# Kernel tuning notes

Hardware: AMD Instinct MI355X
Metric: run time of the kernel (lower is better)

## Reference

```python
import jax, jax.numpy as jnp
import numpy as np

# --- static Cayley table for Cl(3) (8 blades) ---
def _derive_cayley_table():
    basis_gens = [(), (1,), (2,), (3,), (1, 2), (1, 3), (2, 3), (1, 2, 3)]
    gens_to_idx = {g: i for i, g in enumerate(basis_gens)}
    def reduce(a, b):
        gens = list(a) + list(b)
        sign = 1
        changed = True
        while changed:
            changed = False
            i = 0
            while i < len(gens) - 1:
                if gens[i] == gens[i + 1]:
                    gens.pop(i); gens.pop(i)
                    changed = True
                    if i > 0:
                        i -= 1
                elif gens[i] > gens[i + 1]:
                    gens[i], gens[i + 1] = gens[i + 1], gens[i]
                    sign *= -1
                    changed = True
                    i += 1
                else:
                    i += 1
        return gens_to_idx[tuple(gens)], sign
    return [[reduce(basis_gens[i], basis_gens[j]) for j in range(8)] for i in range(8)]

_TAB = _derive_cayley_table()
SI = np.array([i for i in range(8) for _ in range(8)], dtype=np.int32)
SJ = np.array([j for _ in range(8) for j in range(8)], dtype=np.int32)
TK = np.array([_TAB[i][j][0] for i in range(8) for j in range(8)], dtype=np.int32)
SG = np.array([float(_TAB[i][j][1]) for i in range(8) for j in range(8)], dtype=np.float32)

N_TOK, N_BLADE, D_BLADE, D_FFN = 8192, 8, 256, 1024
LN_EPS = 1e-5


def setup_inputs() -> dict:
    key = jax.random.key(0)
    ks = jax.random.split(key, 5)
    scale = 0.02
    return {
        'x': jax.random.normal(ks[0], (N_TOK, N_BLADE, D_BLADE), jnp.float32),
        'interaction_weights': jnp.full((64,), 0.1, jnp.float32),
        'geo_gate': jnp.asarray(0.5, jnp.float32),
        'ln_w': jnp.ones((D_BLADE,), jnp.float32),
        'ln_b': jnp.zeros((D_BLADE,), jnp.float32),
        'W_gate': jax.random.normal(ks[1], (D_BLADE, D_FFN), jnp.float32) * scale,
        'W_up': jax.random.normal(ks[2], (D_BLADE, D_FFN), jnp.float32) * scale,
        'W_down': jax.random.normal(ks[3], (D_FFN, D_BLADE), jnp.float32) * scale,
    }


def reference(x, interaction_weights, geo_gate, ln_w, ln_b, W_gate, W_up, W_down):
    si = jnp.asarray(SI); sj = jnp.asarray(SJ); tk = jnp.asarray(TK)
    sg = jnp.asarray(SG).astype(x.dtype)
    w = jax.nn.sigmoid(interaction_weights).astype(x.dtype)
    # gather blade pairs, weighted Cayley product: (N, 64, D)
    products = x[:, si, :] * x[:, sj, :] * (sg * w)[None, :, None]
    # scatter-add into target blades: (N, 8, D)
    geo = jnp.zeros_like(x).at[:, tk, :].add(products)
    g = jax.nn.sigmoid(geo_gate)
    mixed = g * geo + (1.0 - g) * x
    # LayerNorm over D
    flat = mixed.reshape(-1, x.shape[-1])
    mu = jnp.mean(flat, axis=-1, keepdims=True)
    var = jnp.var(flat, axis=-1, keepdims=True)
    flat = (flat - mu) * jax.lax.rsqrt(var + LN_EPS) * ln_w + ln_b
    # SwiGLU FFN
    h = jax.nn.silu(flat @ W_gate) * (flat @ W_up)
    out = (h @ W_down).reshape(x.shape)
    return x + out
```

## Files before the change

### kernel.cpp

```cpp
#include <hip/hip_runtime.h>
#include <hip/hip_bf16.h>

typedef __bf16 bf16x8 __attribute__((ext_vector_type(8)));
typedef float floatx4 __attribute__((ext_vector_type(4)));

constexpr int TK[64] = {
  0,1,2,3,4,5,6,7,
  1,0,4,5,2,3,7,6,
  2,4,0,6,1,7,3,5,
  3,5,6,0,7,1,2,4,
  4,2,1,7,0,6,5,3,
  5,3,7,1,6,0,4,2,
  6,7,3,2,5,4,0,1,
  7,6,5,4,3,2,1,0
};
constexpr float SGN[64] = {
  1, 1, 1, 1, 1, 1, 1, 1,
  1, 1, 1, 1, 1, 1, 1, 1,
  1,-1, 1, 1,-1,-1, 1,-1,
  1,-1,-1, 1, 1,-1,-1, 1,
  1,-1, 1, 1,-1,-1, 1,-1,
  1,-1,-1, 1, 1,-1,-1, 1,
  1, 1,-1, 1,-1, 1,-1,-1,
  1, 1,-1, 1,-1, 1,-1,-1
};

__device__ __forceinline__ void async16(const void* g, void* l) {
  __builtin_amdgcn_global_load_lds(
      (const __attribute__((address_space(1))) void*)g,
      (__attribute__((address_space(3))) void*)l, 16, 0, 0);
}

__global__ __launch_bounds__(256) void transpose_cast(
    const float* __restrict__ src, __bf16* __restrict__ dst, int K, int N)
{
  __shared__ float s[32 * 33];
  const int t = threadIdx.x;
  const int k0 = blockIdx.y * 32, n0 = blockIdx.x * 32;
  const int r = t >> 5, c = t & 31;
  #pragma unroll
  for (int i = 0; i < 4; ++i)
    s[(r + i * 8) * 33 + c] = src[(size_t)(k0 + r + i * 8) * N + n0 + c];
  __syncthreads();
  #pragma unroll
  for (int i = 0; i < 4; ++i)
    dst[(size_t)(n0 + r + i * 8) * K + k0 + c] = (__bf16)s[c * 33 + r + i * 8];
}

__global__ __launch_bounds__(256) void geo_ln(
    const float* __restrict__ X,
    const float* __restrict__ IW,
    const float* __restrict__ GG,
    const float* __restrict__ LW, const float* __restrict__ LB,
    __bf16* __restrict__ F)
{
  __shared__ float sw[64];
  __shared__ float smix[8 * 256];
  __shared__ float sstat[16];
  const int t = threadIdx.x;
  const int tok = blockIdx.x;

  if (t < 64) sw[t] = SGN[t] / (1.f + __expf(-IW[t]));

  float xv[8];
  #pragma unroll
  for (int b = 0; b < 8; ++b) xv[b] = X[(size_t)tok * 2048 + b * 256 + t];
  const float g = 1.f / (1.f + __expf(-GG[0]));

  __syncthreads();

  float geo[8] = {0.f, 0.f, 0.f, 0.f, 0.f, 0.f, 0.f, 0.f};
  #pragma unroll
  for (int p = 0; p < 64; ++p)
    geo[TK[p]] += xv[p >> 3] * xv[p & 7] * sw[p];

  float mv[8];
  #pragma unroll
  for (int b = 0; b < 8; ++b) {
    mv[b] = g * geo[b] + (1.f - g) * xv[b];
    smix[b * 256 + t] = mv[b];
  }
  __syncthreads();

  const int wv = t >> 6, lane = t & 63;
  #pragma unroll
  for (int s = 0; s < 2; ++s) {
    int b = wv * 2 + s;
    float v0 = smix[b * 256 + lane];
    float v1 = smix[b * 256 + 64 + lane];
    float v2 = smix[b * 256 + 128 + lane];
    float v3 = smix[b * 256 + 192 + lane];
    float sum = v0 + v1 + v2 + v3;
    float sq  = v0*v0 + v1*v1 + v2*v2 + v3*v3;
    #pragma unroll
    for (int off = 32; off > 0; off >>= 1) {
      sum += __shfl_xor(sum, off, 64);
      sq  += __shfl_xor(sq,  off, 64);
    }
    if (lane == 0) {
      float mu  = sum * (1.f / 256.f);
      float var = sq * (1.f / 256.f) - mu * mu;
      sstat[b]     = mu;
      sstat[8 + b] = rsqrtf(var + 1e-5f);
    }
  }
  __syncthreads();

  const float lw = LW[t], lb = LB[t];
  #pragma unroll
  for (int b = 0; b < 8; ++b) {
    float v = (mv[b] - sstat[b]) * sstat[8 + b] * lw + lb;
    F[(size_t)(tok * 8 + b) * 256 + t] = (__bf16)v;
  }
}

__global__ __launch_bounds__(256, 3) void gemm_gateup(
    const __bf16* __restrict__ A,
    const __bf16* __restrict__ Bg,
    const __bf16* __restrict__ Bu,
    __bf16* __restrict__ H)
{
  __shared__ __bf16 sA[128 * 64];
  __shared__ __bf16 sBg[64 * 64];
  __shared__ __bf16 sBu[64 * 64];
  const int t = threadIdx.x;
  const int f0 = blockIdx.x * 64;
  const int m0 = blockIdx.y * 128;
  const int lane = t & 63, wv = t >> 6;
  const int wm = wv & 1, wf = wv >> 1;
  const int l15 = lane & 15, quad = lane >> 4;

  int aoff[4], boff[2];
  #pragma unroll
  for (int i = 0; i < 4; ++i) {
    int idx = i * 256 + t, row = idx >> 3, slot = idx & 7;
    aoff[i] = (m0 + row) * 256 + (slot ^ (row & 7)) * 8;
  }
  #pragma unroll
  for (int i = 0; i < 2; ++i) {
    int idx = i * 256 + t, row = idx >> 3, slot = idx & 7;
    boff[i] = (f0 + row) * 256 + (slot ^ (row & 7)) * 8;
  }

  floatx4 zero = {0.f, 0.f, 0.f, 0.f};
  floatx4 accg[4][2], accu[4][2];
  #pragma unroll
  for (int i = 0; i < 4; ++i)
    #pragma unroll
    for (int j = 0; j < 2; ++j) { accg[i][j] = zero; accu[i][j] = zero; }

  const int xr = l15 & 7;
  for (int k = 0; k < 4; ++k) {
    const int kk = k * 64;
    #pragma unroll
    for (int i = 0; i < 4; ++i) async16(A + aoff[i] + kk, &sA[(i * 256 + t) * 8]);
    #pragma unroll
    for (int i = 0; i < 2; ++i) {
      async16(Bg + boff[i] + kk, &sBg[(i * 256 + t) * 8]);
      async16(Bu + boff[i] + kk, &sBu[(i * 256 + t) * 8]);
    }
    __syncthreads();

    #pragma unroll
    for (int s = 0; s < 2; ++s) {
      const int slot = (s * 4 + quad) ^ xr;
      bf16x8 av[4], bg[2], bu[2];
      #pragma unroll
      for (int i = 0; i < 4; ++i) {
        int r = wm * 64 + i * 16 + l15;
        av[i] = *(const bf16x8*)&sA[r * 64 + slot * 8];
      }
      #pragma unroll
      for (int j = 0; j < 2; ++j) {
        int r = wf * 32 + j * 16 + l15;
        bg[j] = *(const bf16x8*)&sBg[r * 64 + slot * 8];
        bu[j] = *(const bf16x8*)&sBu[r * 64 + slot * 8];
      }
      #pragma unroll
      for (int i = 0; i < 4; ++i)
        #pragma unroll
        for (int j = 0; j < 2; ++j) {
          accg[i][j] = __builtin_amdgcn_mfma_f32_16x16x32_bf16(av[i], bg[j], accg[i][j], 0, 0, 0);
          accu[i][j] = __builtin_amdgcn_mfma_f32_16x16x32_bf16(av[i], bu[j], accu[i][j], 0, 0, 0);
        }
    }
    __syncthreads();
  }

  #pragma unroll
  for (int i = 0; i < 4; ++i)
    #pragma unroll
    for (int j = 0; j < 2; ++j)
      #pragma unroll
      for (int r = 0; r < 4; ++r) {
        int m = m0 + wm * 64 + i * 16 + quad * 4 + r;
        int f = f0 + wf * 32 + j * 16 + l15;
        float gv = accg[i][j][r];
        float uv = accu[i][j][r];
        float hv = (gv / (1.f + __expf(-gv))) * uv;
        H[(size_t)m * 1024 + f] = (__bf16)hv;
      }
}

__global__ __launch_bounds__(256, 2) void gemm_down(
    const __bf16* __restrict__ A,
    const __bf16* __restrict__ B,
    const float* __restrict__ X,
    float* __restrict__ O)
{
  __shared__ __bf16 sA[128 * 64];
  __shared__ __bf16 sB[256 * 64];
  const int t = threadIdx.x;
  const int m0 = blockIdx.x * 128;
  const int lane = t & 63, wv = t >> 6;
  const int wm = wv & 1, wn = wv >> 1;
  const int l15 = lane & 15, quad = lane >> 4;

  int aoff[4], boff[8];
  #pragma unroll
  for (int i = 0; i < 4; ++i) {
    int idx = i * 256 + t, row = idx >> 3, slot = idx & 7;
    aoff[i] = (m0 + row) * 1024 + (slot ^ (row & 7)) * 8;
  }
  #pragma unroll
  for (int i = 0; i < 8; ++i) {
    int idx = i * 256 + t, row = idx >> 3, slot = idx & 7;
    boff[i] = row * 1024 + (slot ^ (row & 7)) * 8;
  }

  floatx4 zero = {0.f, 0.f, 0.f, 0.f};
  floatx4 acc[4][8];
  #pragma unroll
  for (int i = 0; i < 4; ++i)
    #pragma unroll
    for (int j = 0; j < 8; ++j) acc[i][j] = zero;

  const int xr = l15 & 7;
  for (int k = 0; k < 16; ++k) {
    const int kk = k * 64;
    #pragma unroll
    for (int i = 0; i < 4; ++i) async16(A + aoff[i] + kk, &sA[(i * 256 + t) * 8]);
    #pragma unroll
    for (int i = 0; i < 8; ++i) async16(B + boff[i] + kk, &sB[(i * 256 + t) * 8]);
    __syncthreads();

    #pragma unroll
    for (int s = 0; s < 2; ++s) {
      const int slot = (s * 4 + quad) ^ xr;
      bf16x8 av[4], bv[8];
      #pragma unroll
      for (int i = 0; i < 4; ++i) {
        int r = wm * 64 + i * 16 + l15;
        av[i] = *(const bf16x8*)&sA[r * 64 + slot * 8];
      }
      #pragma unroll
      for (int j = 0; j < 8; ++j) {
        int r = wn * 128 + j * 16 + l15;
        bv[j] = *(const bf16x8*)&sB[r * 64 + slot * 8];
      }
      #pragma unroll
      for (int i = 0; i < 4; ++i)
        #pragma unroll
        for (int j = 0; j < 8; ++j)
          acc[i][j] = __builtin_amdgcn_mfma_f32_16x16x32_bf16(av[i], bv[j], acc[i][j], 0, 0, 0);
    }
    __syncthreads();
  }

  #pragma unroll
  for (int i = 0; i < 4; ++i)
    #pragma unroll
    for (int j = 0; j < 8; ++j)
      #pragma unroll
      for (int r = 0; r < 4; ++r) {
        int m = m0 + wm * 64 + i * 16 + quad * 4 + r;
        int n = wn * 128 + j * 16 + l15;
        size_t o = (size_t)m * 256 + n;
        O[o] = X[o] + acc[i][j][r];
      }
}

extern "C" void kernel_launch(void* const* d_in, const int* in_sizes, int n_in,
                              void* d_out, int out_size, void* d_ws, size_t ws_size,
                              hipStream_t stream) {
  const float* x   = (const float*)d_in[0];
  const float* iw  = (const float*)d_in[1];
  const float* gg  = (const float*)d_in[2];
  const float* lnw = (const float*)d_in[3];
  const float* lnb = (const float*)d_in[4];
  const float* Wg  = (const float*)d_in[5];
  const float* Wu  = (const float*)d_in[6];
  const float* Wd  = (const float*)d_in[7];
  float* out = (float*)d_out;

  char* ws = (char*)d_ws;
  __bf16* flat = (__bf16*)(ws);
  __bf16* h    = (__bf16*)(ws + 33554432);
  __bf16* Bg   = (__bf16*)(ws + 167772160);
  __bf16* Bu   = (__bf16*)(ws + 168296448);
  __bf16* Bd   = (__bf16*)(ws + 168820736);

  transpose_cast<<<dim3(32, 8),  256, 0, stream>>>(Wg, Bg, 256, 1024);
  transpose_cast<<<dim3(32, 8),  256, 0, stream>>>(Wu, Bu, 256, 1024);
  transpose_cast<<<dim3(8, 32),  256, 0, stream>>>(Wd, Bd, 1024, 256);
  geo_ln<<<8192, 256, 0, stream>>>(x, iw, gg, lnw, lnb, flat);
  gemm_gateup<<<dim3(16, 512), 256, 0, stream>>>(flat, Bg, Bu, h);
  gemm_down<<<512, 256, 0, stream>>>(h, Bd, x, out);
}
```

Before: 286.8 us.

## Store SwiGLU hidden and down weights in FP8, widen gate/up tile

```diff
diff --git a/kernel.cpp b/kernel.cpp
--- a/kernel.cpp
+++ b/kernel.cpp
@@ -1,5 +1,6 @@
 #include <hip/hip_runtime.h>
 #include <hip/hip_bf16.h>
+#include <hip/hip_fp8.h>
 
 typedef __bf16 bf16x8 __attribute__((ext_vector_type(8)));
 typedef float floatx4 __attribute__((ext_vector_type(4)));
@@ -31,6 +32,11 @@
       (__attribute__((address_space(3))) void*)l, 16, 0, 0);
 }
 
+__device__ __forceinline__ unsigned char to_fp8(float v) {
+  __hip_fp8_e4m3 q(v);
+  return (unsigned char)q.__x;
+}
+
 __global__ __launch_bounds__(256) void transpose_cast(
     const float* __restrict__ src, __bf16* __restrict__ dst, int K, int N)
 {
@@ -45,6 +51,22 @@
   #pragma unroll
   for (int i = 0; i < 4; ++i)
     dst[(size_t)(n0 + r + i * 8) * K + k0 + c] = (__bf16)s[c * 33 + r + i * 8];
+}
+
+__global__ __launch_bounds__(256) void transpose_cast_fp8(
+    const float* __restrict__ src, unsigned char* __restrict__ dst, int K, int N)
+{
+  __shared__ float s[32 * 33];
+  const int t = threadIdx.x;
+  const int k0 = blockIdx.y * 32, n0 = blockIdx.x * 32;
+  const int r = t >> 5, c = t & 31;
+  #pragma unroll
+  for (int i = 0; i < 4; ++i)
+    s[(r + i * 8) * 33 + c] = src[(size_t)(k0 + r + i * 8) * N + n0 + c];
+  __syncthreads();
+  #pragma unroll
+  for (int i = 0; i < 4; ++i)
+    dst[(size_t)(n0 + r + i * 8) * K + k0 + c] = to_fp8(16.f * s[c * 33 + r + i * 8]);
 }
 
 __global__ __launch_bounds__(256) void geo_ln(
@@ -114,48 +136,43 @@
   }
 }
 
-__global__ __launch_bounds__(256, 3) void gemm_gateup(
+__global__ __launch_bounds__(256, 2) void gemm_gateup(
     const __bf16* __restrict__ A,
     const __bf16* __restrict__ Bg,
     const __bf16* __restrict__ Bu,
-    __bf16* __restrict__ H)
+    unsigned char* __restrict__ H)
 {
   __shared__ __bf16 sA[128 * 64];
-  __shared__ __bf16 sBg[64 * 64];
-  __shared__ __bf16 sBu[64 * 64];
-  const int t = threadIdx.x;
-  const int f0 = blockIdx.x * 64;
+  __shared__ __bf16 sBg[128 * 64];
+  __shared__ __bf16 sBu[128 * 64];
+  const int t = threadIdx.x;
+  const int f0 = blockIdx.x * 128;
   const int m0 = blockIdx.y * 128;
   const int lane = t & 63, wv = t >> 6;
   const int wm = wv & 1, wf = wv >> 1;
   const int l15 = lane & 15, quad = lane >> 4;
 
-  int aoff[4], boff[2];
+  int aoff[4], boff[4];
   #pragma unroll
   for (int i = 0; i < 4; ++i) {
     int idx = i * 256 + t, row = idx >> 3, slot = idx & 7;
     aoff[i] = (m0 + row) * 256 + (slot ^ (row & 7)) * 8;
-  }
-  #pragma unroll
-  for (int i = 0; i < 2; ++i) {
-    int idx = i * 256 + t, row = idx >> 3, slot = idx & 7;
     boff[i] = (f0 + row) * 256 + (slot ^ (row & 7)) * 8;
   }
 
   floatx4 zero = {0.f, 0.f, 0.f, 0.f};
-  floatx4 accg[4][2], accu[4][2];
-  #pragma unroll
-  for (int i = 0; i < 4; ++i)
-    #pragma unroll
-    for (int j = 0; j < 2; ++j) { accg[i][j] = zero; accu[i][j] = zero; }
+  floatx4 accg[4][4], accu[4][4];
+  #pragma unroll
+  for (int i = 0; i < 4; ++i)
+    #pragma unroll
+    for (int j = 0; j < 4; ++j) { accg[i][j] = zero; accu[i][j] = zero; }
 
   const int xr = l15 & 7;
   for (int k = 0; k < 4; ++k) {
     const int kk = k * 64;
     #pragma unroll
-    for (int i = 0; i < 4; ++i) async16(A + aoff[i] + kk, &sA[(i * 256 + t) * 8]);
-    #pragma unroll
-    for (int i = 0; i < 2; ++i) {
+    for (int i = 0; i < 4; ++i) {
+      async16(A  + aoff[i] + kk, &sA[(i * 256 + t) * 8]);
       async16(Bg + boff[i] + kk, &sBg[(i * 256 + t) * 8]);
       async16(Bu + boff[i] + kk, &sBu[(i * 256 + t) * 8]);
     }
@@ -164,22 +181,22 @@
     #pragma unroll
     for (int s = 0; s < 2; ++s) {
       const int slot = (s * 4 + quad) ^ xr;
-      bf16x8 av[4], bg[2], bu[2];
+      bf16x8 av[4], bg[4], bu[4];
       #pragma unroll
       for (int i = 0; i < 4; ++i) {
         int r = wm * 64 + i * 16 + l15;
         av[i] = *(const bf16x8*)&sA[r * 64 + slot * 8];
       }
       #pragma unroll
-      for (int j = 0; j < 2; ++j) {
-        int r = wf * 32 + j * 16 + l15;
+      for (int j = 0; j < 4; ++j) {
+        int r = wf * 64 + j * 16 + l15;
         bg[j] = *(const bf16x8*)&sBg[r * 64 + slot * 8];
         bu[j] = *(const bf16x8*)&sBu[r * 64 + slot * 8];
       }
       #pragma unroll
       for (int i = 0; i < 4; ++i)
         #pragma unroll
-        for (int j = 0; j < 2; ++j) {
+        for (int j = 0; j < 4; ++j) {
           accg[i][j] = __builtin_amdgcn_mfma_f32_16x16x32_bf16(av[i], bg[j], accg[i][j], 0, 0, 0);
           accu[i][j] = __builtin_amdgcn_mfma_f32_16x16x32_bf16(av[i], bu[j], accu[i][j], 0, 0, 0);
         }
@@ -190,42 +207,42 @@
   #pragma unroll
   for (int i = 0; i < 4; ++i)
     #pragma unroll
-    for (int j = 0; j < 2; ++j)
+    for (int j = 0; j < 4; ++j)
       #pragma unroll
       for (int r = 0; r < 4; ++r) {
         int m = m0 + wm * 64 + i * 16 + quad * 4 + r;
-        int f = f0 + wf * 32 + j * 16 + l15;
+        int f = f0 + wf * 64 + j * 16 + l15;
         float gv = accg[i][j][r];
         float uv = accu[i][j][r];
         float hv = (gv / (1.f + __expf(-gv))) * uv;
-        H[(size_t)m * 1024 + f] = (__bf16)hv;
-      }
-}
-
-__global__ __launch_bounds__(256, 2) void gemm_down(
-    const __bf16* __restrict__ A,
-    const __bf16* __restrict__ B,
+        H[(size_t)m * 1024 + f] = to_fp8(16.f * hv);
+      }
+}
+
+__global__ __launch_bounds__(256, 3) void gemm_down(
+    const unsigned char* __restrict__ A,
+    const unsigned char* __restrict__ B,
     const float* __restrict__ X,
     float* __restrict__ O)
 {
-  __shared__ __bf16 sA[128 * 64];
-  __shared__ __bf16 sB[256 * 64];
+  __shared__ unsigned char sA[128 * 64];
+  __shared__ unsigned char sB[256 * 64];
   const int t = threadIdx.x;
   const int m0 = blockIdx.x * 128;
   const int lane = t & 63, wv = t >> 6;
   const int wm = wv & 1, wn = wv >> 1;
   const int l15 = lane & 15, quad = lane >> 4;
 
-  int aoff[4], boff[8];
+  int aoff[2], boff[4];
+  #pragma unroll
+  for (int i = 0; i < 2; ++i) {
+    int idx = i * 256 + t, row = idx >> 2, q = idx & 3;
+    aoff[i] = (m0 + row) * 1024 + (q ^ ((row >> 1) & 3)) * 16;
+  }
   #pragma unroll
   for (int i = 0; i < 4; ++i) {
-    int idx = i * 256 + t, row = idx >> 3, slot = idx & 7;
-    aoff[i] = (m0 + row) * 1024 + (slot ^ (row & 7)) * 8;
-  }
-  #pragma unroll
-  for (int i = 0; i < 8; ++i) {
-    int idx = i * 256 + t, row = idx >> 3, slot = idx & 7;
-    boff[i] = row * 1024 + (slot ^ (row & 7)) * 8;
+    int idx = i * 256 + t, row = idx >> 2, q = idx & 3;
+    boff[i] = row * 1024 + (q ^ ((row >> 1) & 3)) * 16;
   }
 
   floatx4 zero = {0.f, 0.f, 0.f, 0.f};
@@ -235,34 +252,35 @@
     #pragma unroll
     for (int j = 0; j < 8; ++j) acc[i][j] = zero;
 
-  const int xr = l15 & 7;
   for (int k = 0; k < 16; ++k) {
     const int kk = k * 64;
     #pragma unroll
-    for (int i = 0; i < 4; ++i) async16(A + aoff[i] + kk, &sA[(i * 256 + t) * 8]);
-    #pragma unroll
-    for (int i = 0; i < 8; ++i) async16(B + boff[i] + kk, &sB[(i * 256 + t) * 8]);
+    for (int i = 0; i < 2; ++i) async16(A + aoff[i] + kk, &sA[(i * 256 + t) * 16]);
+    #pragma unroll
+    for (int i = 0; i < 4; ++i) async16(B + boff[i] + kk, &sB[(i * 256 + t) * 16]);
     __syncthreads();
 
     #pragma unroll
     for (int s = 0; s < 2; ++s) {
-      const int slot = (s * 4 + quad) ^ xr;
-      bf16x8 av[4], bv[8];
+      const int u = s * 4 + quad;
+      long av[4], bv[8];
       #pragma unroll
       for (int i = 0; i < 4; ++i) {
         int r = wm * 64 + i * 16 + l15;
-        av[i] = *(const bf16x8*)&sA[r * 64 + slot * 8];
+        int byte = r * 64 + (((u >> 1) ^ ((r >> 1) & 3)) << 4) + (u & 1) * 8;
+        av[i] = *(const long*)&sA[byte];
       }
       #pragma unroll
       for (int j = 0; j < 8; ++j) {
         int r = wn * 128 + j * 16 + l15;
-        bv[j] = *(const bf16x8*)&sB[r * 64 + slot * 8];
+        int byte = r * 64 + (((u >> 1) ^ ((r >> 1) & 3)) << 4) + (u & 1) * 8;
+        bv[j] = *(const long*)&sB[byte];
       }
       #pragma unroll
       for (int i = 0; i < 4; ++i)
         #pragma unroll
         for (int j = 0; j < 8; ++j)
-          acc[i][j] = __builtin_amdgcn_mfma_f32_16x16x32_bf16(av[i], bv[j], acc[i][j], 0, 0, 0);
+          acc[i][j] = __builtin_amdgcn_mfma_f32_16x16x32_fp8_fp8(av[i], bv[j], acc[i][j], 0, 0, 0);
     }
     __syncthreads();
   }
@@ -276,7 +294,7 @@
         int m = m0 + wm * 64 + i * 16 + quad * 4 + r;
         int n = wn * 128 + j * 16 + l15;
         size_t o = (size_t)m * 256 + n;
-        O[o] = X[o] + acc[i][j][r];
+        O[o] = X[o] + acc[i][j][r] * (1.f / 256.f);
       }
 }
 
@@ -294,16 +312,16 @@
   float* out = (float*)d_out;
 
   char* ws = (char*)d_ws;
-  __bf16* flat = (__bf16*)(ws);
-  __bf16* h    = (__bf16*)(ws + 33554432);
-  __bf16* Bg   = (__bf16*)(ws + 167772160);
-  __bf16* Bu   = (__bf16*)(ws + 168296448);
-  __bf16* Bd   = (__bf16*)(ws + 168820736);
+  __bf16*        flat = (__bf16*)(ws);
+  unsigned char* h    = (unsigned char*)(ws + 33554432);
+  __bf16*        Bg   = (__bf16*)(ws + 100663296);
+  __bf16*        Bu   = (__bf16*)(ws + 101187584);
+  unsigned char* Bd   = (unsigned char*)(ws + 101711872);
 
   transpose_cast<<<dim3(32, 8),  256, 0, stream>>>(Wg, Bg, 256, 1024);
   transpose_cast<<<dim3(32, 8),  256, 0, stream>>>(Wu, Bu, 256, 1024);
-  transpose_cast<<<dim3(8, 32),  256, 0, stream>>>(Wd, Bd, 1024, 256);
+  transpose_cast_fp8<<<dim3(8, 32), 256, 0, stream>>>(Wd, Bd, 1024, 256);
   geo_ln<<<8192, 256, 0, stream>>>(x, iw, gg, lnw, lnb, flat);
-  gemm_gateup<<<dim3(16, 512), 256, 0, stream>>>(flat, Bg, Bu, h);
+  gemm_gateup<<<dim3(8, 512), 256, 0, stream>>>(flat, Bg, Bu, h);
   gemm_down<<<512, 256, 0, stream>>>(h, Bd, x, out);
 }
```

New measurement: 318.6 us. +11.1%, slower.
